# Performance work log

Measured on AMD Instinct MI355X. Metric: run time of the kernel, lower is better.

The kernel has to match this reference:

```python
import jax, jax.numpy as jnp
import numpy as np

VL = 32

def setup_inputs() -> dict:
    key = jax.random.key(0)
    k1, k2, k3 = jax.random.split(key, 3)
    user = jax.random.normal(k1, (16384, 20, VL + 1), dtype=jnp.float32)
    ctx = jax.random.normal(k2, (16384, 10, VL + 1), dtype=jnp.float32)
    doc = jax.random.normal(k3, (16384, 30, VL + 1), dtype=jnp.float32)
    return {"user": user, "ctx": ctx, "doc": doc}

def reference(user, ctx, doc):
    # feats: [B, F, vl+1] where F = total field count across user/ctx/doc
    feats = jnp.concatenate([user, ctx, doc], axis=1)
    v = feats[..., :VL]          # [B, F, vl] latent factors
    linear = feats[..., -1]      # [B, F]   linear term (last column)
    # FM cross term: 0.5 * ((sum_f v)^2 - sum_f v^2), summed over latent dims
    sum_v = jnp.sum(v, axis=1)           # [B, vl]
    sum_v2 = jnp.sum(v * v, axis=1)      # [B, vl]
    cross = 0.5 * jnp.sum(sum_v * sum_v - sum_v2, axis=-1)  # [B]
    logits = cross + jnp.sum(linear, axis=1)                 # [B]
    return jax.nn.sigmoid(logits)
```

## Files before the change

### kernel.cpp

```cpp
#include <hip/hip_runtime.h>
#include <hip/hip_bf16.h>
#include <math.h>


#define NS 16384

__global__ __launch_bounds__(128) void fm_kernel(
    const float* __restrict__ user,
    const float* __restrict__ ctx,
    const float* __restrict__ doc,
    float* __restrict__ out) {
  __shared__ float smem[3960];

  const int tid = threadIdx.x;
  const int spair = blockIdx.x * 2;

  const float4* gu = (const float4*)(user + (size_t)spair * 660);
  const float4* gc = (const float4*)(ctx  + (size_t)spair * 330);
  const float4* gd = (const float4*)(doc  + (size_t)spair * 990);
  float4* su = (float4*)smem;
  float4* sc = (float4*)(smem + 1320);
  float4* sd = (float4*)(smem + 1980);

  {
    float4 r0 = gu[tid], r1 = gu[128 + tid];
    float4 r2, r3, r4, r5, r6, r7;
    bool pu = (256 + tid) < 330;
    if (pu) r2 = gu[256 + tid];
    r3 = gc[tid];
    bool pc = (128 + tid) < 165;
    if (pc) r4 = gc[128 + tid];
    r5 = gd[tid];
    r6 = gd[128 + tid];
    r7 = gd[256 + tid];
    bool pd = (384 + tid) < 495;
    float4 r8;
    if (pd) r8 = gd[384 + tid];

    su[tid] = r0;
    su[128 + tid] = r1;
    if (pu) su[256 + tid] = r2;
    sc[tid] = r3;
    if (pc) sc[128 + tid] = r4;
    sd[tid] = r5;
    sd[128 + tid] = r6;
    sd[256 + tid] = r7;
    if (pd) sd[384 + tid] = r8;
  }
  __syncthreads();

  const int w = tid >> 6;
  const int l = tid & 63;
  const int h = l >> 5;
  const int e = l & 31;

  const float* mu = smem + w * 660;
  const float* mc = smem + 1320 + w * 330;
  const float* md = smem + 1980 + w * 990;

  const float* p1 = (h ? md : mu) + e;
  const float* p2 = (h ? (md + 660) : mc) + e;

  float sv = 0.f, sv2 = 0.f;
#pragma unroll
  for (int f = 0; f < 20; ++f) {
    float x = p1[f * 33];
    sv += x; sv2 = fmaf(x, x, sv2);
  }
#pragma unroll
  for (int f = 0; f < 10; ++f) {
    float x = p2[f * 33];
    sv += x; sv2 = fmaf(x, x, sv2);
  }

  float lin = 0.f;
  if (h == 0) {
    if (e < 20)      lin = mu[e * 33 + 32];
    else if (e < 30) lin = mc[(e - 20) * 33 + 32];
  } else {
    if (e < 30)      lin = md[e * 33 + 32];
  }

  float svT  = sv  + __shfl_xor(sv,  32, 64);
  float sv2T = sv2 + __shfl_xor(sv2, 32, 64);
  float linT = lin + __shfl_xor(lin, 32, 64);

  float part = fmaf(svT, svT, -sv2T);

#pragma unroll
  for (int m = 16; m > 0; m >>= 1) {
    part += __shfl_xor(part, m, 64);
    linT += __shfl_xor(linT, m, 64);
  }

  if (l == 0) {
    float logit = fmaf(0.5f, part, linT);
    out[spair + w] = 1.f / (1.f + expf(-logit));
  }
}

extern "C" void kernel_launch(void* const* d_in, const int* in_sizes, int n_in,
                              void* d_out, int out_size, void* d_ws, size_t ws_size,
                              hipStream_t stream) {
  const float* user = (const float*)d_in[0];
  const float* ctx  = (const float*)d_in[1];
  const float* doc  = (const float*)d_in[2];
  float* out = (float*)d_out;

  dim3 block(128);
  dim3 grid(NS / 2);
  fm_kernel<<<grid, block, 0, stream>>>(user, ctx, doc, out);
}
```

Measured before the change: 142.6 us.

## Process four sample pairs per block with register-prefetched next tile

Each block now loops over four sample pairs instead of one. While the current pair is reduced from shared memory, the next pair's data is loaded from global memory into registers, then written to shared memory between barriers. This aims to overlap global load latency with compute and cut the block count. The cost is a quarter as many blocks, more registers held live for the prefetch, and two extra barriers per iteration.

After: 144.9 us. About the same (+1.6%).

```diff
diff --git a/kernel.cpp b/kernel.cpp
--- a/kernel.cpp
+++ b/kernel.cpp
@@ -4,6 +4,7 @@
 
 
 #define NS 16384
+#define PPB 4
 
 __global__ __launch_bounds__(128) void fm_kernel(
     const float* __restrict__ user,
@@ -13,30 +14,33 @@
   __shared__ float smem[3960];
 
   const int tid = threadIdx.x;
-  const int spair = blockIdx.x * 2;
+  const int pair0 = blockIdx.x * PPB;
 
-  const float4* gu = (const float4*)(user + (size_t)spair * 660);
-  const float4* gc = (const float4*)(ctx  + (size_t)spair * 330);
-  const float4* gd = (const float4*)(doc  + (size_t)spair * 990);
   float4* su = (float4*)smem;
   float4* sc = (float4*)(smem + 1320);
   float4* sd = (float4*)(smem + 1980);
 
-  {
-    float4 r0 = gu[tid], r1 = gu[128 + tid];
-    float4 r2, r3, r4, r5, r6, r7;
-    bool pu = (256 + tid) < 330;
+  const bool pu = (256 + tid) < 330;
+  const bool pc = (128 + tid) < 165;
+  const bool pd = (384 + tid) < 495;
+
+  float4 r0, r1, r2, r3, r4, r5, r6, r7, r8;
+
+  auto LOAD = [&](int pair) {
+    const float4* gu = (const float4*)(user + (size_t)(2 * pair) * 660);
+    const float4* gc = (const float4*)(ctx  + (size_t)(2 * pair) * 330);
+    const float4* gd = (const float4*)(doc  + (size_t)(2 * pair) * 990);
+    r0 = gu[tid];
+    r1 = gu[128 + tid];
     if (pu) r2 = gu[256 + tid];
     r3 = gc[tid];
-    bool pc = (128 + tid) < 165;
     if (pc) r4 = gc[128 + tid];
     r5 = gd[tid];
     r6 = gd[128 + tid];
     r7 = gd[256 + tid];
-    bool pd = (384 + tid) < 495;
-    float4 r8;
     if (pd) r8 = gd[384 + tid];
-
+  };
+  auto STORE = [&]() {
     su[tid] = r0;
     su[128 + tid] = r1;
     if (pu) su[256 + tid] = r2;
@@ -46,7 +50,10 @@
     sd[128 + tid] = r6;
     sd[256 + tid] = r7;
     if (pd) sd[384 + tid] = r8;
-  }
+  };
+
+  LOAD(pair0);
+  STORE();
   __syncthreads();
 
   const int w = tid >> 6;
@@ -57,45 +64,52 @@
   const float* mu = smem + w * 660;
   const float* mc = smem + 1320 + w * 330;
   const float* md = smem + 1980 + w * 990;
-
   const float* p1 = (h ? md : mu) + e;
   const float* p2 = (h ? (md + 660) : mc) + e;
 
-  float sv = 0.f, sv2 = 0.f;
+  for (int it = 0; it < PPB; ++it) {
+    const bool more = (it + 1 < PPB);
+    if (more) LOAD(pair0 + it + 1);
+
+    float sv = 0.f, sv2 = 0.f;
 #pragma unroll
-  for (int f = 0; f < 20; ++f) {
-    float x = p1[f * 33];
-    sv += x; sv2 = fmaf(x, x, sv2);
-  }
+    for (int f = 0; f < 20; ++f) {
+      float x = p1[f * 33];
+      sv += x; sv2 = fmaf(x, x, sv2);
+    }
 #pragma unroll
-  for (int f = 0; f < 10; ++f) {
-    float x = p2[f * 33];
-    sv += x; sv2 = fmaf(x, x, sv2);
-  }
+    for (int f = 0; f < 10; ++f) {
+      float x = p2[f * 33];
+      sv += x; sv2 = fmaf(x, x, sv2);
+    }
 
-  float lin = 0.f;
-  if (h == 0) {
-    if (e < 20)      lin = mu[e * 33 + 32];
-    else if (e < 30) lin = mc[(e - 20) * 33 + 32];
-  } else {
-    if (e < 30)      lin = md[e * 33 + 32];
-  }
+    float lin = 0.f;
+    if (h == 0) {
+      if (e < 20)      lin = mu[e * 33 + 32];
+      else if (e < 30) lin = mc[(e - 20) * 33 + 32];
+    } else {
+      if (e < 30) lin = md[e * 33 + 32];
+    }
 
-  float svT  = sv  + __shfl_xor(sv,  32, 64);
-  float sv2T = sv2 + __shfl_xor(sv2, 32, 64);
-  float linT = lin + __shfl_xor(lin, 32, 64);
+    float svT  = sv  + __shfl_xor(sv,  32, 64);
+    float sv2T = sv2 + __shfl_xor(sv2, 32, 64);
+    float linT = lin + __shfl_xor(lin, 32, 64);
+    float part = fmaf(svT, svT, -sv2T);
+#pragma unroll
+    for (int m = 16; m > 0; m >>= 1) {
+      part += __shfl_xor(part, m, 64);
+      linT += __shfl_xor(linT, m, 64);
+    }
+    if (l == 0) {
+      float logit = fmaf(0.5f, part, linT);
+      out[2 * (pair0 + it) + w] = 1.f / (1.f + expf(-logit));
+    }
 
-  float part = fmaf(svT, svT, -sv2T);
-
-#pragma unroll
-  for (int m = 16; m > 0; m >>= 1) {
-    part += __shfl_xor(part, m, 64);
-    linT += __shfl_xor(linT, m, 64);
-  }
-
-  if (l == 0) {
-    float logit = fmaf(0.5f, part, linT);
-    out[spair + w] = 1.f / (1.f + expf(-logit));
+    if (more) {
+      __syncthreads();
+      STORE();
+      __syncthreads();
+    }
   }
 }
 
@@ -108,6 +122,6 @@
   float* out = (float*)d_out;
 
   dim3 block(128);
-  dim3 grid(NS / 2);
+  dim3 grid(NS / 2 / PPB);
   fm_kernel<<<grid, block, 0, stream>>>(user, ctx, doc, out);
 }
```
